# Performance work log

Measured on AMD Instinct MI355X. Metric: run time of the kernel, lower is better.

Reference implementation:

```python
import jax, jax.numpy as jnp
import numpy as np

EMBED_DIM = 1024
NUM_HEADS = 16
HEAD_DIM = EMBED_DIM // NUM_HEADS
FF_DIM = 4 * EMBED_DIM
LN_EPS = 1e-5


def _layernorm(x, g, b):
    mu = jnp.mean(x, axis=-1, keepdims=True)
    var = jnp.var(x, axis=-1, keepdims=True)
    return (x - mu) * jax.lax.rsqrt(var + LN_EPS) * g + b


def setup_inputs() -> dict:
    key = jax.random.key(0)
    ks = jax.random.split(key, 8)
    B, T, C = 2, 2048, EMBED_DIM
    s_c = 1.0 / np.sqrt(C)
    s_f = 1.0 / np.sqrt(FF_DIM)
    return {
        "x": jax.random.normal(ks[0], (B, T, C), jnp.float32),
        "ln1_g": jnp.ones((C,), jnp.float32),
        "ln1_b": jnp.zeros((C,), jnp.float32),
        "qkv_w": jax.random.uniform(ks[1], (C, 3 * C), jnp.float32, -s_c, s_c),
        "qkv_b": jnp.zeros((3 * C,), jnp.float32),
        "out_w": jax.random.uniform(ks[2], (C, C), jnp.float32, -s_c, s_c),
        "out_b": jnp.zeros((C,), jnp.float32),
        "ln2_g": jnp.ones((C,), jnp.float32),
        "ln2_b": jnp.zeros((C,), jnp.float32),
        "ff1_w": jax.random.uniform(ks[3], (C, FF_DIM), jnp.float32, -s_c, s_c),
        "ff1_b": jnp.zeros((FF_DIM,), jnp.float32),
        "ff2_w": jax.random.uniform(ks[4], (FF_DIM, C), jnp.float32, -s_f, s_f),
        "ff2_b": jnp.zeros((C,), jnp.float32),
    }


def reference(x, ln1_g, ln1_b, qkv_w, qkv_b, out_w, out_b,
              ln2_g, ln2_b, ff1_w, ff1_b, ff2_w, ff2_b):
    B, T, C = x.shape
    H, D = NUM_HEADS, HEAD_DIM

    # --- pre-LN causal self-attention ---
    h = _layernorm(x, ln1_g, ln1_b)
    qkv = h @ qkv_w + qkv_b                      # [B,T,3C]
    q, k, v = jnp.split(qkv, 3, axis=-1)
    q = q.reshape(B, T, H, D)
    k = k.reshape(B, T, H, D)
    v = v.reshape(B, T, H, D)
    scores = jnp.einsum('bqhd,bkhd->bhqk', q, k) / np.sqrt(D)  # [B,H,T,T]
    causal = jnp.tril(jnp.ones((T, T), bool))
    scores = jnp.where(causal, scores, -jnp.inf)
    attn = jax.nn.softmax(scores, axis=-1)
    o = jnp.einsum('bhqk,bkhd->bqhd', attn, v).reshape(B, T, C)
    x = x + o @ out_w + out_b

    # --- GELU MLP ---
    h2 = _layernorm(x, ln2_g, ln2_b)
    ff = jax.nn.gelu(h2 @ ff1_w + ff1_b, approximate=False) @ ff2_w + ff2_b
    return x + ff
```

## Files before the change

### kernel.cpp

```cpp
#include <hip/hip_runtime.h>
#include <hip/hip_bf16.h>
#include <math.h>

#define B_ 2
#define T_ 2048
#define C_ 1024
#define H_ 16
#define D_ 64
#define F_ 4096
#define BT_ (B_*T_)

typedef __attribute__((ext_vector_type(8))) short bf16x8;
typedef __attribute__((ext_vector_type(4))) float f32x4;

__device__ __forceinline__ float bfraw2f(unsigned int u){
    union { unsigned int i; float f; } c; c.i = u << 16; return c.f;
}
__device__ __forceinline__ short f2bfraw(float f){
    union { float f; unsigned int i; } c; c.f = f;
    unsigned int u = c.i;
    u += 0x7fffu + ((u >> 16) & 1u);
    return (short)(u >> 16);
}
__device__ __forceinline__ void gl2lds16(const void* g, void* l) {
    __builtin_amdgcn_global_load_lds(
        (const __attribute__((address_space(1))) unsigned int*)g,
        (__attribute__((address_space(3))) unsigned int*)l,
        16, 0, 0);
}

__global__ __launch_bounds__(256) void wconv_all(const float* qkv_w, short* qkvwT,
                                                 const float* out_w, short* outwT,
                                                 const float* ff1_w, short* ff1wT,
                                                 const float* ff2_w, short* ff2wT)
{
    int id = blockIdx.x;
    const float* W; short* Wt; int K, N;
    if (id < 768)       { W = qkv_w; Wt = qkvwT; K = C_; N = 3 * C_; }
    else if (id < 1024) { id -= 768;  W = out_w; Wt = outwT; K = C_; N = C_; }
    else if (id < 2048) { id -= 1024; W = ff1_w; Wt = ff1wT; K = C_; N = F_; }
    else                { id -= 2048; W = ff2_w; Wt = ff2wT; K = F_; N = C_; }
    int ntile = N >> 6;
    int n0 = (id % ntile) * 64, k0 = (id / ntile) * 64;

    __shared__ short tile[64][65];
    int t = threadIdx.x;
#pragma unroll
    for (int i = 0; i < 4; i++) {
        int idx = t + i * 256;
        int r = idx >> 4, c4 = (idx & 15) * 4;
        float4 u = *(const float4*)(W + (size_t)(k0 + r) * N + n0 + c4);
        tile[c4 + 0][r] = f2bfraw(u.x);
        tile[c4 + 1][r] = f2bfraw(u.y);
        tile[c4 + 2][r] = f2bfraw(u.z);
        tile[c4 + 3][r] = f2bfraw(u.w);
    }
    __syncthreads();
#pragma unroll
    for (int i = 0; i < 2; i++) {
        int idx = t + i * 256;
        int r = idx >> 3, c8 = (idx & 7) * 8;
        short v[8];
#pragma unroll
        for (int u8 = 0; u8 < 8; u8++) v[u8] = tile[r][c8 + u8];
        *(uint4*)(Wt + (size_t)(n0 + r) * K + k0 + c8) = *(const uint4*)v;
    }
}

__global__ __launch_bounds__(256) void v_transpose(const __hip_bfloat16* __restrict__ qkv,
                                                   short* __restrict__ vt)
{
    __shared__ short tile[64][65];
    int kb = blockIdx.x * 64;
    int h = blockIdx.y, b = blockIdx.z;
    const short* src = (const short*)qkv + (size_t)b * T_ * 3 * C_ + 2 * C_ + h * D_;
    int t = threadIdx.x;
#pragma unroll
    for (int i = 0; i < 2; i++) {
        int idx = t + i * 256;
        int r = idx >> 3, c8 = (idx & 7) * 8;
        bf16x8 v = *(const bf16x8*)(src + (size_t)(kb + r) * 3 * C_ + c8);
#pragma unroll
        for (int u = 0; u < 8; u++) tile[c8 + u][r] = v[u];
    }
    __syncthreads();
    short* dst = vt + (size_t)(b * H_ + h) * D_ * T_ + kb;
#pragma unroll
    for (int i = 0; i < 2; i++) {
        int idx = t + i * 256;
        int r = idx >> 3, c8 = (idx & 7) * 8;
        short v[8];
#pragma unroll
        for (int u = 0; u < 8; u++) v[u] = tile[r][c8 + u];
        *(uint4*)(dst + (size_t)r * T_ + c8) = *(const uint4*)v;
    }
}

__global__ __launch_bounds__(256) void ln_fused(const float* __restrict__ x, int ldx,
                                                const float* __restrict__ g,
                                                const float* __restrict__ b,
                                                __hip_bfloat16* out, int ldo)
{
    __shared__ float sm1[4], sm2[4];
    __shared__ float smu, srs;
    int row = blockIdx.x, t = threadIdx.x;
    const float* xr = x + (size_t)row * ldx;
    float v[4]; float s = 0.f, ss = 0.f;
#pragma unroll
    for (int i = 0; i < 4; i++) {
        float f = xr[t + i * 256];
        v[i] = f; s += f; ss += f * f;
    }
#pragma unroll
    for (int off = 32; off >= 1; off >>= 1) {
        s  += __shfl_xor(s,  off);
        ss += __shfl_xor(ss, off);
    }
    int wave = t >> 6, lane = t & 63;
    if (!lane) { sm1[wave] = s; sm2[wave] = ss; }
    __syncthreads();
    if (t == 0) {
        s  = sm1[0] + sm1[1] + sm1[2] + sm1[3];
        ss = sm2[0] + sm2[1] + sm2[2] + sm2[3];
        float mu  = s * (1.f / C_);
        float var = ss * (1.f / C_) - mu * mu;
        if (var < 0.f) var = 0.f;
        smu = mu; srs = rsqrtf(var + 1e-5f);
    }
    __syncthreads();
    float mu = smu, rs = srs;
#pragma unroll
    for (int i = 0; i < 4; i++) {
        int c = t + i * 256;
        out[(size_t)row * ldo + c] = __float2bfloat16((v[i] - mu) * rs * g[c] + b[c]);
    }
}

template<int ACT>
__global__ __launch_bounds__(256) void gemm128(
    const __hip_bfloat16* A, int lda,
    const short* Wt, int ldw, int noff, int koff,
    const float* __restrict__ bias, int boff,
    void* out, int ldo,
    int K)
{
    __shared__ __align__(16) short As[3][128 * 32];
    __shared__ __align__(16) short Bs[3][128 * 32];
    int tid = threadIdx.x;
    int w = tid >> 6, lane = tid & 63;
    int quad = lane >> 4, l16 = lane & 15;
    int wm = w >> 1, wn = w & 1;
    int m0 = blockIdx.y * 128, n0 = blockIdx.x * 128;
    int lr = lane >> 2, lk = (lane & 3) * 8;

    const __hip_bfloat16* Ag = A + (size_t)(m0 + w * 32 + lr) * lda + lk;
    const short*          Bg = Wt + (size_t)(noff + n0 + w * 32 + lr) * ldw + koff + lk;

    f32x4 acc[4][4];
#pragma unroll
    for (int i = 0; i < 4; i++)
#pragma unroll
        for (int j = 0; j < 4; j++) acc[i][j] = (f32x4){0.f, 0.f, 0.f, 0.f};

    const int NT = K >> 5;
    {
        gl2lds16(Ag,            &As[0][(w * 32) * 32]);
        gl2lds16(Ag + 16 * lda, &As[0][(w * 32 + 16) * 32]);
        gl2lds16(Bg,            &Bs[0][(w * 32) * 32]);
        gl2lds16(Bg + 16 * ldw, &Bs[0][(w * 32 + 16) * 32]);
        if (NT > 1) {
            gl2lds16(Ag + 32,            &As[1][(w * 32) * 32]);
            gl2lds16(Ag + 16 * lda + 32, &As[1][(w * 32 + 16) * 32]);
            gl2lds16(Bg + 32,            &Bs[1][(w * 32) * 32]);
            gl2lds16(Bg + 16 * ldw + 32, &Bs[1][(w * 32 + 16) * 32]);
        }
    }

    int cur = 0;
    for (int t = 0; t < NT; t++) {
        if (t + 2 < NT) {
            int sb = cur + 2; if (sb >= 3) sb -= 3;
            int ko = (t + 2) << 5;
            gl2lds16(Ag + ko,            &As[sb][(w * 32) * 32]);
            gl2lds16(Ag + 16 * lda + ko, &As[sb][(w * 32 + 16) * 32]);
            gl2lds16(Bg + ko,            &Bs[sb][(w * 32) * 32]);
            gl2lds16(Bg + 16 * ldw + ko, &Bs[sb][(w * 32 + 16) * 32]);
        }
        int ahead = NT - 1 - t;
        if (ahead >= 2)      asm volatile("s_waitcnt vmcnt(8)" ::: "memory");
        else if (ahead == 1) asm volatile("s_waitcnt vmcnt(4)" ::: "memory");
        else                 asm volatile("s_waitcnt vmcnt(0)" ::: "memory");
        __builtin_amdgcn_s_barrier();
        __builtin_amdgcn_sched_barrier(0);

        bf16x8 af[4], bfr[4];
#pragma unroll
        for (int mt = 0; mt < 4; mt++)
            af[mt] = *(const bf16x8*)&As[cur][(wm * 64 + mt * 16 + l16) * 32 + quad * 8];
#pragma unroll
        for (int nt = 0; nt < 4; nt++)
            bfr[nt] = *(const bf16x8*)&Bs[cur][(wn * 64 + nt * 16 + l16) * 32 + quad * 8];
#pragma unroll
        for (int mt = 0; mt < 4; mt++)
#pragma unroll
            for (int nt = 0; nt < 4; nt++)
                acc[mt][nt] = __builtin_amdgcn_mfma_f32_16x16x32_bf16(af[mt], bfr[nt], acc[mt][nt], 0, 0, 0);

        __builtin_amdgcn_sched_barrier(0);
        __builtin_amdgcn_s_barrier();
        cur = (cur == 2) ? 0 : cur + 1;
    }

#pragma unroll
    for (int nt = 0; nt < 4; nt++) {
        int c = n0 + wn * 64 + nt * 16 + l16;
        float bv = bias ? bias[boff + c] : 0.f;
#pragma unroll
        for (int mt = 0; mt < 4; mt++) {
#pragma unroll
            for (int reg = 0; reg < 4; reg++) {
                int r = m0 + wm * 64 + mt * 16 + quad * 4 + reg;
                float v = acc[mt][nt][reg] + bv;
                if (ACT == 1) v = 0.5f * v * (1.f + erff(v * 0.70710678118654752f));
                ((__hip_bfloat16*)out)[(size_t)r * ldo + c] = __float2bfloat16(v);
            }
        }
    }
}

__global__ __launch_bounds__(256) void gemm64n(
    const __hip_bfloat16* A, int lda,
    const short* Wt, int ldw, int koff,
    const float* __restrict__ bias,
    const float* res, int ldres,
    float* out, int ldo,
    int K)
{
    __shared__ __align__(16) short As[3][128 * 32];
    __shared__ __align__(16) short Bs[3][64 * 32];
    int tid = threadIdx.x;
    int w = tid >> 6, lane = tid & 63;
    int quad = lane >> 4, l16 = lane & 15;
    int wm = w >> 1, wn = w & 1;
    int m0 = blockIdx.y * 128, n0 = blockIdx.x * 64;
    int lr = lane >> 2, lk = (lane & 3) * 8;

    const __hip_bfloat16* Ag = A + (size_t)(m0 + w * 32 + lr) * lda + lk;
    const short*          Bg = Wt + (size_t)(n0 + w * 16 + lr) * ldw + koff + lk;

    f32x4 acc[4][2];
#pragma unroll
    for (int i = 0; i < 4; i++)
#pragma unroll
        for (int j = 0; j < 2; j++) acc[i][j] = (f32x4){0.f, 0.f, 0.f, 0.f};

    const int NT = K >> 5;
    {
        gl2lds16(Ag,            &As[0][(w * 32) * 32]);
        gl2lds16(Ag + 16 * lda, &As[0][(w * 32 + 16) * 32]);
        gl2lds16(Bg,            &Bs[0][(w * 16) * 32]);
        if (NT > 1) {
            gl2lds16(Ag + 32,            &As[1][(w * 32) * 32]);
            gl2lds16(Ag + 16 * lda + 32, &As[1][(w * 32 + 16) * 32]);
            gl2lds16(Bg + 32,            &Bs[1][(w * 16) * 32]);
        }
    }

    int cur = 0;
    for (int t = 0; t < NT; t++) {
        if (t + 2 < NT) {
            int sb = cur + 2; if (sb >= 3) sb -= 3;
            int ko = (t + 2) << 5;
            gl2lds16(Ag + ko,            &As[sb][(w * 32) * 32]);
            gl2lds16(Ag + 16 * lda + ko, &As[sb][(w * 32 + 16) * 32]);
            gl2lds16(Bg + ko,            &Bs[sb][(w * 16) * 32]);
        }
        int ahead = NT - 1 - t;
        if (ahead >= 2)      asm volatile("s_waitcnt vmcnt(6)" ::: "memory");
        else if (ahead == 1) asm volatile("s_waitcnt vmcnt(3)" ::: "memory");
        else                 asm volatile("s_waitcnt vmcnt(0)" ::: "memory");
        __builtin_amdgcn_s_barrier();
        __builtin_amdgcn_sched_barrier(0);

        bf16x8 af[4], bfr[2];
#pragma unroll
        for (int mt = 0; mt < 4; mt++)
            af[mt] = *(const bf16x8*)&As[cur][(wm * 64 + mt * 16 + l16) * 32 + quad * 8];
#pragma unroll
        for (int nt = 0; nt < 2; nt++)
            bfr[nt] = *(const bf16x8*)&Bs[cur][(wn * 32 + nt * 16 + l16) * 32 + quad * 8];
#pragma unroll
        for (int mt = 0; mt < 4; mt++)
#pragma unroll
            for (int nt = 0; nt < 2; nt++)
                acc[mt][nt] = __builtin_amdgcn_mfma_f32_16x16x32_bf16(af[mt], bfr[nt], acc[mt][nt], 0, 0, 0);

        __builtin_amdgcn_sched_barrier(0);
        __builtin_amdgcn_s_barrier();
        cur = (cur == 2) ? 0 : cur + 1;
    }

#pragma unroll
    for (int nt = 0; nt < 2; nt++) {
        int c = n0 + wn * 32 + nt * 16 + l16;
        float bv = bias ? bias[c] : 0.f;
#pragma unroll
        for (int mt = 0; mt < 4; mt++) {
#pragma unroll
            for (int reg = 0; reg < 4; reg++) {
                int r = m0 + wm * 64 + mt * 16 + quad * 4 + reg;
                float v = acc[mt][nt][reg] + bv + res[(size_t)r * ldres + c];
                out[(size_t)r * ldo + c] = v;
            }
        }
    }
}

__global__ __launch_bounds__(256, 2) void attn_flash(__hip_bfloat16* qkv,
                                                     const short* __restrict__ vt)
{
    __shared__ __align__(16) short Ks[2][2][64 * 64];
    __shared__ __align__(16) short Vs[2][2][64 * 64];
    __shared__ __align__(16) short Pl[4][16 * 72];
    int tid = threadIdx.x;
    int wave = tid >> 6, lane = tid & 63;
    int quad = lane >> 4, l16 = lane & 15;
    int fid = blockIdx.x + 16 * blockIdx.y;
    int h = (fid & 7) * 2 + ((fid >> 3) >> 4);
    int i = (fid >> 3) & 15;
    int b = blockIdx.z;
    int qbs[2]; qbs[0] = i; qbs[1] = 31 - i;
    const size_t rs = 3 * C_;
    __hip_bfloat16* base = qkv + (size_t)b * T_ * rs;
    const __hip_bfloat16* Qb = base + h * D_;
    const __hip_bfloat16* Kb = base + C_ + h * D_;
    const short* Vt = vt + (size_t)(b * H_ + h) * D_ * T_;

    bf16x8 qf[2][2];
#pragma unroll
    for (int tq = 0; tq < 2; tq++) {
        const __hip_bfloat16* qr = Qb + (size_t)(qbs[tq] * 64 + wave * 16 + l16) * rs + quad * 8;
        qf[tq][0] = *(const bf16x8*)qr;
        qf[tq][1] = *(const bf16x8*)(qr + 32);
    }

    f32x4 o[2][4];
    float m[2][4], l[2][4];
#pragma unroll
    for (int tq = 0; tq < 2; tq++)
#pragma unroll
        for (int t = 0; t < 4; t++) {
            o[tq][t] = (f32x4){0.f, 0.f, 0.f, 0.f};
            m[tq][t] = -INFINITY;
            l[tq][t] = 0.f;
        }
    short* Pw = &Pl[wave][0];

    int srow = wave * 16 + (lane >> 3);
    int scg  = ((lane & 7) ^ (lane >> 3)) * 8;
    const __hip_bfloat16* Kg = Kb + (size_t)srow * rs + scg;
    const short*          Vg = Vt + (size_t)srow * T_ + scg;

    int qhi = qbs[1];
    int NS = (qhi >> 1) + 1;
    int swz = (l16 & 7);
    int cur = 0;

#pragma unroll
    for (int sub = 0; sub < 2; sub++)
#pragma unroll
        for (int j = 0; j < 2; j++) {
            gl2lds16(Kg + (size_t)(sub * 64 + j * 8) * rs, &Ks[0][sub][(wave * 2 + j) * 512]);
            gl2lds16(Vg + (size_t)(j * 8) * T_ + sub * 64, &Vs[0][sub][(wave * 2 + j) * 512]);
        }
    __syncthreads();

    for (int s = 0; s < NS; s++) {
        if (s + 1 < NS) {
            int kb = (s + 1) * 128;
#pragma unroll
            for (int sub = 0; sub < 2; sub++)
#pragma unroll
                for (int j = 0; j < 2; j++) {
                    gl2lds16(Kg + (size_t)(kb + sub * 64 + j * 8) * rs, &Ks[cur ^ 1][sub][(wave * 2 + j) * 512]);
                    gl2lds16(Vg + (size_t)(j * 8) * T_ + kb + sub * 64, &Vs[cur ^ 1][sub][(wave * 2 + j) * 512]);
                }
        }
#pragma unroll
        for (int sub = 0; sub < 2; sub++) {
            int kt = 2 * s + sub;
            if (kt > qhi) break;
            const short* Kc = Ks[cur][sub];
            const short* Vc = Vs[cur][sub];
#pragma unroll
            for (int tq = 0; tq < 2; tq++) {
                if (kt > qbs[tq]) continue;
                f32x4 sa[4];
                __builtin_amdgcn_s_setprio(1);
#pragma unroll
                for (int t16 = 0; t16 < 4; t16++) {
                    int row = t16 * 16 + l16;
                    bf16x8 kf0 = *(const bf16x8*)&Kc[row * 64 + ((quad     ^ swz)) * 8];
                    bf16x8 kf1 = *(const bf16x8*)&Kc[row * 64 + (((quad + 4) ^ swz)) * 8];
                    f32x4 sv = (f32x4){0.f, 0.f, 0.f, 0.f};
                    sv = __builtin_amdgcn_mfma_f32_16x16x32_bf16(qf[tq][0], kf0, sv, 0, 0, 0);
                    sv = __builtin_amdgcn_mfma_f32_16x16x32_bf16(qf[tq][1], kf1, sv, 0, 0, 0);
                    sa[t16] = sv;
                }
                __builtin_amdgcn_s_setprio(0);
                bool maskit = (kt == qbs[tq]);
#pragma unroll
                for (int t16 = 0; t16 < 4; t16++) {
#pragma unroll
                    for (int reg = 0; reg < 4; reg++) {
                        float v = sa[t16][reg] * 0.125f;
                        if (maskit) {
                            int keyl = t16 * 16 + l16;
                            int ql = wave * 16 + quad * 4 + reg;
                            if (keyl > ql) v = -3.0e38f;
                        }
                        sa[t16][reg] = v;
                    }
                }
                float mx[4];
#pragma unroll
                for (int reg = 0; reg < 4; reg++)
                    mx[reg] = fmaxf(fmaxf(sa[0][reg], sa[1][reg]), fmaxf(sa[2][reg], sa[3][reg]));
#pragma unroll
                for (int off = 8; off >= 1; off >>= 1)
#pragma unroll
                    for (int reg = 0; reg < 4; reg++)
                        mx[reg] = fmaxf(mx[reg], __shfl_xor(mx[reg], off));
                float alpha[4];
#pragma unroll
                for (int reg = 0; reg < 4; reg++) {
                    float mn = fmaxf(m[tq][reg], mx[reg]);
                    alpha[reg] = __expf(m[tq][reg] - mn);
                    m[tq][reg] = mn;
                }
                float rsum[4] = {0.f, 0.f, 0.f, 0.f};
#pragma unroll
                for (int t16 = 0; t16 < 4; t16++) {
#pragma unroll
                    for (int reg = 0; reg < 4; reg++) {
                        float p = __expf(sa[t16][reg] - m[tq][reg]);
                        rsum[reg] += p;
                        Pw[(quad * 4 + reg) * 72 + t16 * 16 + l16] = f2bfraw(p);
                    }
                }
#pragma unroll
                for (int off = 8; off >= 1; off >>= 1)
#pragma unroll
                    for (int reg = 0; reg < 4; reg++)
                        rsum[reg] += __shfl_xor(rsum[reg], off);
#pragma unroll
                for (int reg = 0; reg < 4; reg++)
                    l[tq][reg] = l[tq][reg] * alpha[reg] + rsum[reg];
#pragma unroll
                for (int t = 0; t < 4; t++)
#pragma unroll
                    for (int reg = 0; reg < 4; reg++)
                        o[tq][t][reg] *= alpha[reg];
                __builtin_amdgcn_s_setprio(1);
#pragma unroll
                for (int chunk = 0; chunk < 2; chunk++) {
                    bf16x8 pf = *(const bf16x8*)&Pw[l16 * 72 + chunk * 32 + quad * 8];
#pragma unroll
                    for (int dt = 0; dt < 4; dt++) {
                        int row = dt * 16 + l16;
                        bf16x8 vf = *(const bf16x8*)&Vc[row * 64 + (((chunk * 4 + quad) ^ swz)) * 8];
                        o[tq][dt] = __builtin_amdgcn_mfma_f32_16x16x32_bf16(pf, vf, o[tq][dt], 0, 0, 0);
                    }
                }
                __builtin_amdgcn_s_setprio(0);
            }
        }
        __syncthreads();
        cur ^= 1;
    }

#pragma unroll
    for (int tq = 0; tq < 2; tq++) {
#pragma unroll
        for (int dt = 0; dt < 4; dt++) {
#pragma unroll
            for (int reg = 0; reg < 4; reg++) {
                int r = qbs[tq] * 64 + wave * 16 + quad * 4 + reg;
                float v = o[tq][dt][reg] / l[tq][reg];
                base[(size_t)r * rs + h * D_ + dt * 16 + l16] = __float2bfloat16(v);
            }
        }
    }
}

extern "C" void kernel_launch(void* const* d_in, const int* in_sizes, int n_in,
                              void* d_out, int out_size, void* d_ws, size_t ws_size,
                              hipStream_t stream)
{
    const float* x     = (const float*)d_in[0];
    const float* ln1_g = (const float*)d_in[1];
    const float* ln1_b = (const float*)d_in[2];
    const float* qkv_w = (const float*)d_in[3];
    const float* qkv_b = (const float*)d_in[4];
    const float* out_w = (const float*)d_in[5];
    const float* out_b = (const float*)d_in[6];
    const float* ln2_g = (const float*)d_in[7];
    const float* ln2_b = (const float*)d_in[8];
    const float* ff1_w = (const float*)d_in[9];
    const float* ff1_b = (const float*)d_in[10];
    const float* ff2_w = (const float*)d_in[11];
    const float* ff2_b = (const float*)d_in[12];

    char* ws = (char*)d_ws;
    __hip_bfloat16* qkv = (__hip_bfloat16*)ws;
    short* qkvwT = (short*)(ws + 25165824);
    short* outwT = (short*)(ws + 31457280);
    short* ff1wT = (short*)(ws + 33554432);
    short* ff2wT = (short*)(ws + 41943040);
    __hip_bfloat16* hbuf2 = qkv;
    __hip_bfloat16* act   = qkv + 1024;
    __hip_bfloat16* hbuf1 = (__hip_bfloat16*)d_out;
    float* x1 = (float*)d_out;
    short* vtbuf = (short*)d_out;

    wconv_all<<<3072, 256, 0, stream>>>(qkv_w, qkvwT, out_w, outwT,
                                        ff1_w, ff1wT, ff2_w, ff2wT);

    ln_fused<<<BT_, 256, 0, stream>>>(x, C_, ln1_g, ln1_b, hbuf1, C_);
    gemm128<0><<<dim3(3 * C_ / 128, BT_ / 128), 256, 0, stream>>>(
        hbuf1, C_, qkvwT, C_, 0, 0, qkv_b, 0, qkv, 3 * C_, C_);
    v_transpose<<<dim3(T_ / 64, H_, B_), 256, 0, stream>>>(qkv, vtbuf);
    attn_flash<<<dim3(16, H_, B_), 256, 0, stream>>>(qkv, vtbuf);
    gemm64n<<<dim3(C_ / 64, BT_ / 128), 256, 0, stream>>>(
        qkv, 3 * C_, outwT, C_, 0, out_b, x, C_, x1, C_, C_);
    ln_fused<<<BT_, 256, 0, stream>>>(x1, C_, ln2_g, ln2_b, hbuf2, 3 * C_);
    for (int f = 0; f < 2; f++) {
        gemm128<1><<<dim3(2048 / 128, BT_ / 128), 256, 0, stream>>>(
            hbuf2, 3 * C_, ff1wT, C_, f * 2048, 0, ff1_b, f * 2048,
            act, 3 * C_, C_);
        gemm64n<<<dim3(C_ / 64, BT_ / 128), 256, 0, stream>>>(
            act, 3 * C_, ff2wT, F_, f * 2048, (f == 0 ? ff2_b : nullptr),
            x1, C_, x1, C_, 2048);
    }
}
```

Before: 425.4 us.

## Unify GEMMs into 512-thread 256x128 tile kernel with BK=64 and swizzled LDS

Replaces the two GEMM kernels (128x128 and 128x64 tiles) with one 8-wave kernel that computes 256x128 output tiles and steps K by 64 per stage. The shared-memory layout is XOR-swizzled to avoid bank conflicts, there is one barrier per stage instead of two, and s_setprio is raised around the MFMA blocks. The residual-add epilogue becomes a template variant. Larger tiles and fewer barriers aim to improve data reuse and MFMA utilisation. The cost is about 147KB of LDS per block, so only one block fits per CU, and the N=1024 GEMMs now launch only 128 blocks, which can leave many CUs idle.

Result: slower. 473.0 us (+11.2%).

```diff
diff --git a/kernel.cpp b/kernel.cpp
--- a/kernel.cpp
+++ b/kernel.cpp
@@ -137,24 +137,27 @@
 }
 
 template<int ACT>
-__global__ __launch_bounds__(256) void gemm128(
+__global__ __launch_bounds__(512, 2) void gemm8p(
     const __hip_bfloat16* A, int lda,
     const short* Wt, int ldw, int noff, int koff,
     const float* __restrict__ bias, int boff,
+    const float* res, int ldres,
     void* out, int ldo,
     int K)
 {
-    __shared__ __align__(16) short As[3][128 * 32];
-    __shared__ __align__(16) short Bs[3][128 * 32];
+    __shared__ __align__(16) short As[3][256 * 64];
+    __shared__ __align__(16) short Bs[3][128 * 64];
     int tid = threadIdx.x;
     int w = tid >> 6, lane = tid & 63;
     int quad = lane >> 4, l16 = lane & 15;
-    int wm = w >> 1, wn = w & 1;
-    int m0 = blockIdx.y * 128, n0 = blockIdx.x * 128;
-    int lr = lane >> 2, lk = (lane & 3) * 8;
-
-    const __hip_bfloat16* Ag = A + (size_t)(m0 + w * 32 + lr) * lda + lk;
-    const short*          Bg = Wt + (size_t)(noff + n0 + w * 32 + lr) * ldw + koff + lk;
+    int wm = w >> 2, wn = w & 3;
+    wm = w >> 1; wn = w & 1;
+    int m0 = blockIdx.y * 256, n0 = blockIdx.x * 128;
+
+    int lane8 = lane >> 3;
+    int cswz  = ((lane & 7) ^ lane8) * 8;
+    const __hip_bfloat16* AgS = A + (size_t)(m0 + w * 32 + lane8) * lda + cswz;
+    const short*          BgS = Wt + (size_t)(noff + n0 + w * 16 + lane8) * ldw + koff + cswz;
 
     f32x4 acc[4][4];
 #pragma unroll
@@ -162,51 +165,59 @@
 #pragma unroll
         for (int j = 0; j < 4; j++) acc[i][j] = (f32x4){0.f, 0.f, 0.f, 0.f};
 
-    const int NT = K >> 5;
-    {
-        gl2lds16(Ag,            &As[0][(w * 32) * 32]);
-        gl2lds16(Ag + 16 * lda, &As[0][(w * 32 + 16) * 32]);
-        gl2lds16(Bg,            &Bs[0][(w * 32) * 32]);
-        gl2lds16(Bg + 16 * ldw, &Bs[0][(w * 32 + 16) * 32]);
-        if (NT > 1) {
-            gl2lds16(Ag + 32,            &As[1][(w * 32) * 32]);
-            gl2lds16(Ag + 16 * lda + 32, &As[1][(w * 32 + 16) * 32]);
-            gl2lds16(Bg + 32,            &Bs[1][(w * 32) * 32]);
-            gl2lds16(Bg + 16 * ldw + 32, &Bs[1][(w * 32 + 16) * 32]);
-        }
-    }
+    const int NT = K >> 6;
+    int swz = (l16 & 7);
+
+#pragma unroll
+    for (int p = 0; p < 2; p++) {
+        int ko = p * 64;
+#pragma unroll
+        for (int j = 0; j < 4; j++)
+            gl2lds16(AgS + (size_t)(j * 8) * lda + ko, &As[p][(w * 4 + j) * 512]);
+#pragma unroll
+        for (int j = 0; j < 2; j++)
+            gl2lds16(BgS + (size_t)(j * 8) * ldw + ko, &Bs[p][(w * 2 + j) * 512]);
+    }
+    __syncthreads();
 
     int cur = 0;
     for (int t = 0; t < NT; t++) {
         if (t + 2 < NT) {
             int sb = cur + 2; if (sb >= 3) sb -= 3;
-            int ko = (t + 2) << 5;
-            gl2lds16(Ag + ko,            &As[sb][(w * 32) * 32]);
-            gl2lds16(Ag + 16 * lda + ko, &As[sb][(w * 32 + 16) * 32]);
-            gl2lds16(Bg + ko,            &Bs[sb][(w * 32) * 32]);
-            gl2lds16(Bg + 16 * ldw + ko, &Bs[sb][(w * 32 + 16) * 32]);
+            int ko = (t + 2) << 6;
+#pragma unroll
+            for (int j = 0; j < 4; j++)
+                gl2lds16(AgS + (size_t)(j * 8) * lda + ko, &As[sb][(w * 4 + j) * 512]);
+#pragma unroll
+            for (int j = 0; j < 2; j++)
+                gl2lds16(BgS + (size_t)(j * 8) * ldw + ko, &Bs[sb][(w * 2 + j) * 512]);
+        }
+        const short* Ac = As[cur];
+        const short* Bc = Bs[cur];
+#pragma unroll
+        for (int h = 0; h < 2; h++) {
+            bf16x8 af[4], bfr[4];
+#pragma unroll
+            for (int mt = 0; mt < 4; mt++) {
+                int row = wm * 64 + mt * 16 + l16;
+                af[mt] = *(const bf16x8*)&Ac[row * 64 + (((h * 4 + quad) ^ swz)) * 8];
+            }
+#pragma unroll
+            for (int nt = 0; nt < 4; nt++) {
+                int row = wn * 64 + nt * 16 + l16;
+                bfr[nt] = *(const bf16x8*)&Bc[row * 64 + (((h * 4 + quad) ^ swz)) * 8];
+            }
+            __builtin_amdgcn_s_setprio(1);
+#pragma unroll
+            for (int mt = 0; mt < 4; mt++)
+#pragma unroll
+                for (int nt = 0; nt < 4; nt++)
+                    acc[mt][nt] = __builtin_amdgcn_mfma_f32_16x16x32_bf16(af[mt], bfr[nt], acc[mt][nt], 0, 0, 0);
+            __builtin_amdgcn_s_setprio(0);
         }
         int ahead = NT - 1 - t;
-        if (ahead >= 2)      asm volatile("s_waitcnt vmcnt(8)" ::: "memory");
-        else if (ahead == 1) asm volatile("s_waitcnt vmcnt(4)" ::: "memory");
-        else                 asm volatile("s_waitcnt vmcnt(0)" ::: "memory");
-        __builtin_amdgcn_s_barrier();
-        __builtin_amdgcn_sched_barrier(0);
-
-        bf16x8 af[4], bfr[4];
-#pragma unroll
-        for (int mt = 0; mt < 4; mt++)
-            af[mt] = *(const bf16x8*)&As[cur][(wm * 64 + mt * 16 + l16) * 32 + quad * 8];
-#pragma unroll
-        for (int nt = 0; nt < 4; nt++)
-            bfr[nt] = *(const bf16x8*)&Bs[cur][(wn * 64 + nt * 16 + l16) * 32 + quad * 8];
-#pragma unroll
-        for (int mt = 0; mt < 4; mt++)
-#pragma unroll
-            for (int nt = 0; nt < 4; nt++)
-                acc[mt][nt] = __builtin_amdgcn_mfma_f32_16x16x32_bf16(af[mt], bfr[nt], acc[mt][nt], 0, 0, 0);
-
-        __builtin_amdgcn_sched_barrier(0);
+        if (ahead >= 2)      asm volatile("s_waitcnt vmcnt(6)" ::: "memory");
+        else if (ahead == 1) asm volatile("s_waitcnt vmcnt(0)" ::: "memory");
         __builtin_amdgcn_s_barrier();
         cur = (cur == 2) ? 0 : cur + 1;
     }
@@ -222,95 +233,12 @@
                 int r = m0 + wm * 64 + mt * 16 + quad * 4 + reg;
                 float v = acc[mt][nt][reg] + bv;
                 if (ACT == 1) v = 0.5f * v * (1.f + erff(v * 0.70710678118654752f));
-                ((__hip_bfloat16*)out)[(size_t)r * ldo + c] = __float2bfloat16(v);
-            }
-        }
-    }
-}
-
-__global__ __launch_bounds__(256) void gemm64n(
-    const __hip_bfloat16* A, int lda,
-    const short* Wt, int ldw, int koff,
-    const float* __restrict__ bias,
-    const float* res, int ldres,
-    float* out, int ldo,
-    int K)
-{
-    __shared__ __align__(16) short As[3][128 * 32];
-    __shared__ __align__(16) short Bs[3][64 * 32];
-    int tid = threadIdx.x;
-    int w = tid >> 6, lane = tid & 63;
-    int quad = lane >> 4, l16 = lane & 15;
-    int wm = w >> 1, wn = w & 1;
-    int m0 = blockIdx.y * 128, n0 = blockIdx.x * 64;
-    int lr = lane >> 2, lk = (lane & 3) * 8;
-
-    const __hip_bfloat16* Ag = A + (size_t)(m0 + w * 32 + lr) * lda + lk;
-    const short*          Bg = Wt + (size_t)(n0 + w * 16 + lr) * ldw + koff + lk;
-
-    f32x4 acc[4][2];
-#pragma unroll
-    for (int i = 0; i < 4; i++)
-#pragma unroll
-        for (int j = 0; j < 2; j++) acc[i][j] = (f32x4){0.f, 0.f, 0.f, 0.f};
-
-    const int NT = K >> 5;
-    {
-        gl2lds16(Ag,            &As[0][(w * 32) * 32]);
-        gl2lds16(Ag + 16 * lda, &As[0][(w * 32 + 16) * 32]);
-        gl2lds16(Bg,            &Bs[0][(w * 16) * 32]);
-        if (NT > 1) {
-            gl2lds16(Ag + 32,            &As[1][(w * 32) * 32]);
-            gl2lds16(Ag + 16 * lda + 32, &As[1][(w * 32 + 16) * 32]);
-            gl2lds16(Bg + 32,            &Bs[1][(w * 16) * 32]);
-        }
-    }
-
-    int cur = 0;
-    for (int t = 0; t < NT; t++) {
-        if (t + 2 < NT) {
-            int sb = cur + 2; if (sb >= 3) sb -= 3;
-            int ko = (t + 2) << 5;
-            gl2lds16(Ag + ko,            &As[sb][(w * 32) * 32]);
-            gl2lds16(Ag + 16 * lda + ko, &As[sb][(w * 32 + 16) * 32]);
-            gl2lds16(Bg + ko,            &Bs[sb][(w * 16) * 32]);
-        }
-        int ahead = NT - 1 - t;
-        if (ahead >= 2)      asm volatile("s_waitcnt vmcnt(6)" ::: "memory");
-        else if (ahead == 1) asm volatile("s_waitcnt vmcnt(3)" ::: "memory");
-        else                 asm volatile("s_waitcnt vmcnt(0)" ::: "memory");
-        __builtin_amdgcn_s_barrier();
-        __builtin_amdgcn_sched_barrier(0);
-
-        bf16x8 af[4], bfr[2];
-#pragma unroll
-        for (int mt = 0; mt < 4; mt++)
-            af[mt] = *(const bf16x8*)&As[cur][(wm * 64 + mt * 16 + l16) * 32 + quad * 8];
-#pragma unroll
-        for (int nt = 0; nt < 2; nt++)
-            bfr[nt] = *(const bf16x8*)&Bs[cur][(wn * 32 + nt * 16 + l16) * 32 + quad * 8];
-#pragma unroll
-        for (int mt = 0; mt < 4; mt++)
-#pragma unroll
-            for (int nt = 0; nt < 2; nt++)
-                acc[mt][nt] = __builtin_amdgcn_mfma_f32_16x16x32_bf16(af[mt], bfr[nt], acc[mt][nt], 0, 0, 0);
-
-        __builtin_amdgcn_sched_barrier(0);
-        __builtin_amdgcn_s_barrier();
-        cur = (cur == 2) ? 0 : cur + 1;
-    }
-
-#pragma unroll
-    for (int nt = 0; nt < 2; nt++) {
-        int c = n0 + wn * 32 + nt * 16 + l16;
-        float bv = bias ? bias[c] : 0.f;
-#pragma unroll
-        for (int mt = 0; mt < 4; mt++) {
-#pragma unroll
-            for (int reg = 0; reg < 4; reg++) {
-                int r = m0 + wm * 64 + mt * 16 + quad * 4 + reg;
-                float v = acc[mt][nt][reg] + bv + res[(size_t)r * ldres + c];
-                out[(size_t)r * ldo + c] = v;
+                if (ACT == 2) {
+                    v += res[(size_t)r * ldres + c];
+                    ((float*)out)[(size_t)r * ldo + c] = v;
+                } else {
+                    ((__hip_bfloat16*)out)[(size_t)r * ldo + c] = __float2bfloat16(v);
+                }
             }
         }
     }
@@ -527,19 +455,19 @@
                                         ff1_w, ff1wT, ff2_w, ff2wT);
 
     ln_fused<<<BT_, 256, 0, stream>>>(x, C_, ln1_g, ln1_b, hbuf1, C_);
-    gemm128<0><<<dim3(3 * C_ / 128, BT_ / 128), 256, 0, stream>>>(
-        hbuf1, C_, qkvwT, C_, 0, 0, qkv_b, 0, qkv, 3 * C_, C_);
+    gemm8p<0><<<dim3(3 * C_ / 128, BT_ / 256), 512, 0, stream>>>(
+        hbuf1, C_, qkvwT, C_, 0, 0, qkv_b, 0, nullptr, 0, qkv, 3 * C_, C_);
     v_transpose<<<dim3(T_ / 64, H_, B_), 256, 0, stream>>>(qkv, vtbuf);
     attn_flash<<<dim3(16, H_, B_), 256, 0, stream>>>(qkv, vtbuf);
-    gemm64n<<<dim3(C_ / 64, BT_ / 128), 256, 0, stream>>>(
-        qkv, 3 * C_, outwT, C_, 0, out_b, x, C_, x1, C_, C_);
+    gemm8p<2><<<dim3(C_ / 128, BT_ / 256), 512, 0, stream>>>(
+        qkv, 3 * C_, outwT, C_, 0, 0, out_b, 0, x, C_, x1, C_, C_);
     ln_fused<<<BT_, 256, 0, stream>>>(x1, C_, ln2_g, ln2_b, hbuf2, 3 * C_);
     for (int f = 0; f < 2; f++) {
-        gemm128<1><<<dim3(2048 / 128, BT_ / 128), 256, 0, stream>>>(
+        gemm8p<1><<<dim3(2048 / 128, BT_ / 256), 512, 0, stream>>>(
             hbuf2, 3 * C_, ff1wT, C_, f * 2048, 0, ff1_b, f * 2048,
-            act, 3 * C_, C_);
-        gemm64n<<<dim3(C_ / 64, BT_ / 128), 256, 0, stream>>>(
-            act, 3 * C_, ff2wT, F_, f * 2048, (f == 0 ? ff2_b : nullptr),
+            nullptr, 0, act, 3 * C_, C_);
+        gemm8p<2><<<dim3(C_ / 128, BT_ / 256), 512, 0, stream>>>(
+            act, 3 * C_, ff2wT, F_, 0, f * 2048, (f == 0 ? ff2_b : nullptr), 0,
             x1, C_, x1, C_, 2048);
     }
 }
```
